# Kernel optimization log

Measured on AMD Instinct MI355X. Metric: run time of the kernel, lower is better.

Reference implementation:

```python
import jax, jax.numpy as jnp
import numpy as np

N = 50000      # nodes
E = 320000     # edges
D_NODE = 256   # node feature size
D_EDGE = 128   # raw edge feature size
T_DIM = 64     # time encoder out_channels
H = 8          # heads (auto_num_heads(256) -> 8)
C = 32         # per-head dim = 256 // 8
D_E_IN = D_EDGE + T_DIM  # edge_dim into lin_edge


def setup_inputs() -> dict:
    key = jax.random.key(0)
    ks = jax.random.split(key, 16)
    s_n = 1.0 / np.sqrt(D_NODE)
    s_e = 1.0 / np.sqrt(D_E_IN)
    return {
        "edge_tuples": jax.random.randint(ks[0], (2, E), 0, N, dtype=jnp.int64)
        if jax.config.jax_enable_x64 else jax.random.randint(ks[0], (2, E), 0, N),
        "edge_feats": jax.random.normal(ks[1], (E, D_EDGE), jnp.float32),
        "edge_times_rel": jax.random.uniform(ks[2], (E,), jnp.float32) * 100.0,
        "node_feats": jax.random.normal(ks[3], (N, D_NODE), jnp.float32),
        # time encoder: Linear(1, T_DIM) followed by cos
        "w_time": jax.random.normal(ks[4], (T_DIM,), jnp.float32),
        "b_time": jax.random.normal(ks[5], (T_DIM,), jnp.float32),
        # TransformerConv linears (out = H*C = 256)
        "Wq": jax.random.normal(ks[6], (H * C, D_NODE), jnp.float32) * s_n,
        "bq": jnp.zeros((H * C,), jnp.float32),
        "Wk": jax.random.normal(ks[7], (H * C, D_NODE), jnp.float32) * s_n,
        "bk": jnp.zeros((H * C,), jnp.float32),
        "Wv": jax.random.normal(ks[8], (H * C, D_NODE), jnp.float32) * s_n,
        "bv": jnp.zeros((H * C,), jnp.float32),
        "We": jax.random.normal(ks[9], (H * C, D_E_IN), jnp.float32) * s_e,  # lin_edge, no bias
        "Ws": jax.random.normal(ks[10], (H * C, D_NODE), jnp.float32) * s_n,  # lin_skip
        "bs": jnp.zeros((H * C,), jnp.float32),
    }


def reference(edge_tuples, edge_feats, edge_times_rel, node_feats,
              w_time, b_time, Wq, bq, Wk, bk, Wv, bv, We, Ws, bs):
    n_nodes = node_feats.shape[0]
    n_edges = edge_tuples.shape[1]
    src, dst = edge_tuples[0], edge_tuples[1]

    # TGN time encoder: cos(t * w + b)  -> [E, T_DIM]
    tfeat = jnp.cos(edge_times_rel[:, None] * w_time[None, :] + b_time)
    e_attr = jnp.concatenate([tfeat, edge_feats], axis=1)  # [E, T_DIM + D_EDGE]

    # dense per-node projections, then gather per edge
    q = (node_feats @ Wq.T + bq)[dst].reshape(n_edges, H, C)
    k = (node_feats @ Wk.T + bk)[src].reshape(n_edges, H, C)
    v = (node_feats @ Wv.T + bv)[src].reshape(n_edges, H, C)
    ep = (e_attr @ We.T).reshape(n_edges, H, C)

    k = k + ep
    alpha = jnp.sum(q * k, axis=-1) / jnp.sqrt(jnp.asarray(C, q.dtype))  # [E, H]

    # segment softmax over edges grouped by destination node
    m = jax.ops.segment_max(alpha, dst, num_segments=n_nodes)  # [N, H]
    m = jnp.where(jnp.isfinite(m), m, 0.0)
    ea = jnp.exp(alpha - m[dst])
    denom = jax.ops.segment_sum(ea, dst, num_segments=n_nodes)
    a = ea / (denom[dst] + 1e-16)  # [E, H]

    # weighted scatter-aggregate of (value + edge) messages
    msg = a[:, :, None] * (v + ep)  # [E, H, C]
    out = jax.ops.segment_sum(msg, dst, num_segments=n_nodes).reshape(n_nodes, H * C)

    # root / skip connection
    out = out + node_feats @ Ws.T + bs
    return out
```

## Files before the change

### kernel.cpp

```cpp
#include <hip/hip_runtime.h>
#include <hip/hip_bf16.h>
#include <math.h>

#define NN 50000
#define NE 320000
#define SCAN_NBLK ((NN + 255) / 256)

typedef __attribute__((ext_vector_type(8))) short bf16x8;
typedef __attribute__((ext_vector_type(4))) float floatx4;
typedef __attribute__((ext_vector_type(4))) unsigned int uintx4;

static __device__ __forceinline__ unsigned pack2bf(float a, float b) {
    __hip_bfloat162 h = __float22bfloat162_rn(make_float2(a, b));
    return *reinterpret_cast<unsigned*>(&h);
}
static __device__ __forceinline__ unsigned short f2bf(float x) {
    __hip_bfloat16 h = __float2bfloat16(x);
    return *reinterpret_cast<unsigned short*>(&h);
}
static __device__ __forceinline__ float bf2f(unsigned short u) {
    return __uint_as_float(((unsigned)u) << 16);
}
static __device__ __forceinline__ float bflo(unsigned u) {
    return __uint_as_float(u << 16);
}
static __device__ __forceinline__ float bfhi(unsigned u) {
    return __uint_as_float(u & 0xffff0000u);
}
static __device__ __forceinline__ void gload_lds16(const void* g, void* l) {
    __builtin_amdgcn_global_load_lds(
        (const __attribute__((address_space(1))) void*)g,
        (__attribute__((address_space(3))) void*)l, 16, 0, 0);
}

__global__ __launch_bounds__(256)
void cvt_bf16_kernel(const float* __restrict__ in,
                     unsigned short* __restrict__ out, int n8)
{
    int t = blockIdx.x * 256 + threadIdx.x;
    if (t >= n8) return;
    const float4* p = (const float4*)in + (size_t)t * 2;
    float4 a = p[0], b = p[1];
    uint4 u;
    u.x = pack2bf(a.x, a.y); u.y = pack2bf(a.z, a.w);
    u.z = pack2bf(b.x, b.y); u.w = pack2bf(b.z, b.w);
    ((uint4*)out)[t] = u;
}

__global__ __launch_bounds__(256)
void node_gemm_kernel(const unsigned short* __restrict__ Xb,
                      const unsigned short* __restrict__ Wqb,
                      const unsigned short* __restrict__ Wkb,
                      const unsigned short* __restrict__ Wvb,
                      const unsigned short* __restrict__ Wsb,
                      const float* __restrict__ bq, const float* __restrict__ bk,
                      const float* __restrict__ bv, const float* __restrict__ bs,
                      unsigned short* __restrict__ qb,
                      unsigned short* __restrict__ kb,
                      unsigned short* __restrict__ vb,
                      float* __restrict__ outS)
{
    const int m0  = blockIdx.x * 128;
    const int ct  = blockIdx.y;
    const int mat = ct >> 1, half = ct & 1;
    const int colbase = half * 128;

    const unsigned short* __restrict__ W;
    const float* __restrict__ bias;
    switch (mat) {
        case 0:  W = Wqb; bias = bq; break;
        case 1:  W = Wkb; bias = bk; break;
        case 2:  W = Wvb; bias = bv; break;
        default: W = Wsb; bias = bs; break;
    }
    W += (size_t)colbase * 256;

    __shared__ __align__(16) unsigned char smem[32768];
    short* sA = (short*)smem;
    short* sB = (short*)(smem + 16384);

    const int tid  = threadIdx.x;
    const int lane = tid & 63;
    const int wave = tid >> 6;
    const int wm   = (wave & 1) * 64;
    const int wn   = (wave >> 1) * 64;
    const int lr   = lane & 15;
    const int lq   = lane >> 4;

    const int srow = tid >> 3;
    const int scol = (tid & 7) * 8;

    floatx4 acc[4][4];
    #pragma unroll
    for (int i = 0; i < 4; ++i)
        #pragma unroll
        for (int j = 0; j < 4; ++j)
            acc[i][j] = (floatx4){0.f, 0.f, 0.f, 0.f};

    for (int k0 = 0; k0 < 256; k0 += 64) {
        #pragma unroll
        for (int p = 0; p < 4; ++p) {
            int arow = m0 + p * 32 + srow;
            if (arow > NN - 1) arow = NN - 1;
            gload_lds16(Xb + (size_t)arow * 256 + k0 + scol,
                        (char*)sA + p * 4096 + wave * 1024);
            gload_lds16(W + (size_t)(p * 32 + srow) * 256 + k0 + scol,
                        (char*)sB + p * 4096 + wave * 1024);
        }
        __syncthreads();

        #pragma unroll
        for (int ks = 0; ks < 2; ++ks) {
            bf16x8 af[4], bfr[4];
            #pragma unroll
            for (int i = 0; i < 4; ++i)
                af[i] = *(const bf16x8*)&sA[(wm + i * 16 + lr) * 64 + ks * 32 + lq * 8];
            #pragma unroll
            for (int j = 0; j < 4; ++j)
                bfr[j] = *(const bf16x8*)&sB[(wn + j * 16 + lr) * 64 + ks * 32 + lq * 8];
            #pragma unroll
            for (int i = 0; i < 4; ++i)
                #pragma unroll
                for (int j = 0; j < 4; ++j)
                    acc[i][j] = __builtin_amdgcn_mfma_f32_16x16x32_bf16(
                        af[i], bfr[j], acc[i][j], 0, 0, 0);
        }
        __syncthreads();
    }

    if (mat < 3) {
        unsigned short* __restrict__ Cb = (mat == 0) ? qb : (mat == 1) ? kb : vb;
        unsigned short* sOut = (unsigned short*)smem;
        for (int ch = 0; ch < 4; ++ch) {
            __syncthreads();
            if ((ch >> 1) == (wave & 1)) {
                int ibase = (ch & 1) * 2;
                #pragma unroll
                for (int ii = 0; ii < 2; ++ii) {
                    int i = ibase + ii;
                    #pragma unroll
                    for (int j = 0; j < 4; ++j) {
                        int col = wn + j * 16 + lr;
                        float bb = bias[colbase + col];
                        #pragma unroll
                        for (int r = 0; r < 4; ++r) {
                            int rowc = ii * 16 + lq * 4 + r;
                            sOut[rowc * 136 + col] = f2bf(acc[i][j][r] + bb);
                        }
                    }
                }
            }
            __syncthreads();
            #pragma unroll
            for (int p = 0; p < 2; ++p) {
                int rowc = p * 16 + (tid >> 4);
                int off  = (tid & 15) * 8;
                int grow = m0 + ch * 32 + rowc;
                if (grow < NN) {
                    uint4 u = *(const uint4*)&sOut[rowc * 136 + off];
                    *(uint4*)&Cb[(size_t)grow * 256 + colbase + off] = u;
                }
            }
        }
    } else {
        float* sOutF = (float*)smem;
        for (int ch = 0; ch < 8; ++ch) {
            __syncthreads();
            if ((ch >> 2) == (wave & 1)) {
                int i = ch & 3;
                #pragma unroll
                for (int j = 0; j < 4; ++j) {
                    int col = wn + j * 16 + lr;
                    float bb = bias[colbase + col];
                    #pragma unroll
                    for (int r = 0; r < 4; ++r) {
                        int rowc = lq * 4 + r;
                        sOutF[rowc * 132 + col] = acc[i][j][r] + bb;
                    }
                }
            }
            __syncthreads();
            #pragma unroll
            for (int p = 0; p < 2; ++p) {
                int rowc = p * 8 + (tid >> 5);
                int off  = (tid & 31) * 4;
                int grow = m0 + ch * 16 + rowc;
                if (grow < NN) {
                    float4 f = *(const float4*)&sOutF[rowc * 132 + off];
                    *(float4*)&outS[(size_t)grow * 256 + colbase + off] = f;
                }
            }
        }
    }
}

__global__ __launch_bounds__(256)
void edge_gemm_kernel(const float* __restrict__ tvals,
                      const float* __restrict__ w_time,
                      const float* __restrict__ b_time,
                      const float* __restrict__ ef,
                      const unsigned short* __restrict__ Web,
                      unsigned short* __restrict__ epb)
{
    const int m0 = blockIdx.x * 128;
    const int n0 = blockIdx.y * 128;

    __shared__ __align__(16) unsigned char smem[32768];
    short* sA = (short*)smem;
    short* sB = (short*)(smem + 16384);

    const int tid  = threadIdx.x;
    const int lane = tid & 63;
    const int wave = tid >> 6;
    const int wm   = (wave & 1) * 64;
    const int wn   = (wave >> 1) * 64;
    const int lr   = lane & 15;
    const int lq   = lane >> 4;

    const int srow = tid >> 3;
    const int scol = (tid & 7) * 8;

    floatx4 acc[4][4];
    #pragma unroll
    for (int i = 0; i < 4; ++i)
        #pragma unroll
        for (int j = 0; j < 4; ++j)
            acc[i][j] = (floatx4){0.f, 0.f, 0.f, 0.f};

    for (int k0 = 0; k0 < 192; k0 += 64) {
        #pragma unroll
        for (int p = 0; p < 4; ++p)
            gload_lds16(Web + (size_t)(n0 + p * 32 + srow) * 192 + k0 + scol,
                        (char*)sB + p * 4096 + wave * 1024);

        if (k0 == 0) {
            float w8[8], b8[8];
            #pragma unroll
            for (int j = 0; j < 8; ++j) {
                w8[j] = w_time[scol + j];
                b8[j] = b_time[scol + j];
            }
            #pragma unroll
            for (int p = 0; p < 4; ++p) {
                float tvv = tvals[m0 + p * 32 + srow];
                unsigned pk[4];
                #pragma unroll
                for (int j = 0; j < 4; ++j) {
                    float a = cosf(fmaf(tvv, w8[2 * j],     b8[2 * j]));
                    float b = cosf(fmaf(tvv, w8[2 * j + 1], b8[2 * j + 1]));
                    pk[j] = pack2bf(a, b);
                }
                *(uint4*)&sA[p * 2048 + tid * 8] = make_uint4(pk[0], pk[1], pk[2], pk[3]);
            }
        } else {
            float4 f[8];
            #pragma unroll
            for (int p = 0; p < 4; ++p) {
                const float4* src = (const float4*)(ef
                    + (size_t)(m0 + p * 32 + srow) * 128 + (k0 - 64) + scol);
                f[2 * p]     = src[0];
                f[2 * p + 1] = src[1];
            }
            #pragma unroll
            for (int p = 0; p < 4; ++p) {
                uint4 u;
                u.x = pack2bf(f[2 * p].x,     f[2 * p].y);
                u.y = pack2bf(f[2 * p].z,     f[2 * p].w);
                u.z = pack2bf(f[2 * p + 1].x, f[2 * p + 1].y);
                u.w = pack2bf(f[2 * p + 1].z, f[2 * p + 1].w);
                *(uint4*)&sA[p * 2048 + tid * 8] = u;
            }
        }
        __syncthreads();

        #pragma unroll
        for (int ks = 0; ks < 2; ++ks) {
            bf16x8 af[4], bfr[4];
            #pragma unroll
            for (int i = 0; i < 4; ++i)
                af[i] = *(const bf16x8*)&sA[(wm + i * 16 + lr) * 64 + ks * 32 + lq * 8];
            #pragma unroll
            for (int j = 0; j < 4; ++j)
                bfr[j] = *(const bf16x8*)&sB[(wn + j * 16 + lr) * 64 + ks * 32 + lq * 8];
            #pragma unroll
            for (int i = 0; i < 4; ++i)
                #pragma unroll
                for (int j = 0; j < 4; ++j)
                    acc[i][j] = __builtin_amdgcn_mfma_f32_16x16x32_bf16(
                        af[i], bfr[j], acc[i][j], 0, 0, 0);
        }
        __syncthreads();
    }

    unsigned short* sOut = (unsigned short*)smem;
    for (int ch = 0; ch < 4; ++ch) {
        __syncthreads();
        if ((ch >> 1) == (wave & 1)) {
            int ibase = (ch & 1) * 2;
            #pragma unroll
            for (int ii = 0; ii < 2; ++ii) {
                int i = ibase + ii;
                #pragma unroll
                for (int j = 0; j < 4; ++j) {
                    int col = wn + j * 16 + lr;
                    #pragma unroll
                    for (int r = 0; r < 4; ++r) {
                        int rowc = ii * 16 + lq * 4 + r;
                        sOut[rowc * 136 + col] = f2bf(acc[i][j][r]);
                    }
                }
            }
        }
        __syncthreads();
        #pragma unroll
        for (int p = 0; p < 2; ++p) {
            int rowc = p * 16 + (tid >> 4);
            int off  = (tid & 15) * 8;
            int grow = m0 + ch * 32 + rowc;
            uint4 u = *(const uint4*)&sOut[rowc * 136 + off];
            *(uint4*)&epb[(size_t)grow * 256 + n0 + off] = u;
        }
    }
}

__global__ __launch_bounds__(256)
void deg_kernel(const int* __restrict__ et, int* __restrict__ deg)
{
    int e = blockIdx.x * 256 + threadIdx.x;
    if (e < NE) atomicAdd(&deg[et[NE + e]], 1);
}

__global__ __launch_bounds__(256)
void blocksum_kernel(const int* __restrict__ deg, int* __restrict__ bsum)
{
    int idx = blockIdx.x * 256 + threadIdx.x;
    int v = (idx < NN) ? deg[idx] : 0;
    #pragma unroll
    for (int off = 1; off < 64; off <<= 1) v += __shfl_xor(v, off);
    __shared__ int s[4];
    if ((threadIdx.x & 63) == 0) s[threadIdx.x >> 6] = v;
    __syncthreads();
    if (threadIdx.x == 0) bsum[blockIdx.x] = s[0] + s[1] + s[2] + s[3];
}

__global__ __launch_bounds__(256)
void bscan_kernel(int* __restrict__ bsum, int* __restrict__ rowstart)
{
    __shared__ int s[256];
    int t = threadIdx.x;
    int v = (t < SCAN_NBLK) ? bsum[t] : 0;
    s[t] = v;
    __syncthreads();
    #pragma unroll
    for (int off = 1; off < 256; off <<= 1) {
        int u = (t >= off) ? s[t - off] : 0;
        __syncthreads();
        s[t] += u;
        __syncthreads();
    }
    if (t < SCAN_NBLK) bsum[t] = (t == 0) ? 0 : s[t - 1];
    if (t == 0) rowstart[NN] = s[SCAN_NBLK - 1];
}

__global__ __launch_bounds__(256)
void chunkscan_kernel(const int* __restrict__ deg, const int* __restrict__ bsum,
                      int* __restrict__ rowstart, int* __restrict__ cursor)
{
    __shared__ int s[256];
    int t = threadIdx.x;
    int idx = blockIdx.x * 256 + t;
    int v = (idx < NN) ? deg[idx] : 0;
    s[t] = v;
    __syncthreads();
    #pragma unroll
    for (int off = 1; off < 256; off <<= 1) {
        int u = (t >= off) ? s[t - off] : 0;
        __syncthreads();
        s[t] += u;
        __syncthreads();
    }
    if (idx < NN) {
        int ex = bsum[blockIdx.x] + s[t] - v;
        rowstart[idx] = ex;
        cursor[idx]   = ex;
    }
}

__global__ __launch_bounds__(256)
void scatter_kernel(const int* __restrict__ et,
                    int* __restrict__ cursor,
                    int2* __restrict__ eslist)
{
    int e = blockIdx.x * 256 + threadIdx.x;
    if (e < NE) {
        int d   = et[NE + e];
        int pos = atomicAdd(&cursor[d], 1);
        eslist[pos] = make_int2(e, et[e]);
    }
}

static __device__ __forceinline__ void edge_proc(
    uint4 ku, uint4 vu, uintx4 eu, const float* q, float mask,
    float* a, float& accd)
{
    float pe0 = bflo(eu[0]), pe1 = bfhi(eu[0]);
    float pe2 = bflo(eu[1]), pe3 = bfhi(eu[1]);
    float pe4 = bflo(eu[2]), pe5 = bfhi(eu[2]);
    float pe6 = bflo(eu[3]), pe7 = bfhi(eu[3]);

    float part;
    part = q[0] * (bflo(ku.x) + pe0);
    part = fmaf(q[1], bfhi(ku.x) + pe1, part);
    part = fmaf(q[2], bflo(ku.y) + pe2, part);
    part = fmaf(q[3], bfhi(ku.y) + pe3, part);
    part = fmaf(q[4], bflo(ku.z) + pe4, part);
    part = fmaf(q[5], bfhi(ku.z) + pe5, part);
    part = fmaf(q[6], bflo(ku.w) + pe6, part);
    part = fmaf(q[7], bfhi(ku.w) + pe7, part);
    part += __shfl_xor(part, 1);
    part += __shfl_xor(part, 2);

    float ea = __expf(part * 0.17677669529663687f) * mask;

    a[0] = fmaf(ea, bflo(vu.x) + pe0, a[0]);
    a[1] = fmaf(ea, bfhi(vu.x) + pe1, a[1]);
    a[2] = fmaf(ea, bflo(vu.y) + pe2, a[2]);
    a[3] = fmaf(ea, bfhi(vu.y) + pe3, a[3]);
    a[4] = fmaf(ea, bflo(vu.z) + pe4, a[4]);
    a[5] = fmaf(ea, bfhi(vu.z) + pe5, a[5]);
    a[6] = fmaf(ea, bflo(vu.w) + pe6, a[6]);
    a[7] = fmaf(ea, bfhi(vu.w) + pe7, a[7]);
    accd += ea;
}

__global__ __launch_bounds__(256)
void fused_agg_kernel(const int2* __restrict__ eslist,
                      const int* __restrict__ rowstart,
                      const unsigned short* __restrict__ qb,
                      const unsigned short* __restrict__ kb,
                      const unsigned short* __restrict__ vb,
                      const unsigned short* __restrict__ epb,
                      float* __restrict__ out)
{
    const int n = blockIdx.x * 4 + (threadIdx.x >> 6);
    if (n >= NN) return;
    const int lane = threadIdx.x & 63;
    const int half = lane >> 5;
    const int co   = (lane & 31) * 8;

    uint4 qu = *(const uint4*)(qb + (size_t)n * 256 + co);
    float q[8] = { bflo(qu.x), bfhi(qu.x), bflo(qu.y), bfhi(qu.y),
                   bflo(qu.z), bfhi(qu.z), bflo(qu.w), bfhi(qu.w) };

    float a[8] = {0.f, 0.f, 0.f, 0.f, 0.f, 0.f, 0.f, 0.f};
    float accd = 0.f;

    const int s0 = rowstart[n];
    const int s1 = rowstart[n + 1];

    int i = s0;
    for (; i + 4 <= s1; i += 4) {
        const int2 pA = eslist[i + half];
        const int2 pB = eslist[i + 2 + half];
        uint4 kA = *(const uint4*)(kb + (size_t)pA.y * 256 + co);
        uint4 vA = *(const uint4*)(vb + (size_t)pA.y * 256 + co);
        uintx4 eA = __builtin_nontemporal_load(
                        (const uintx4*)(epb + (size_t)pA.x * 256 + co));
        uint4 kB = *(const uint4*)(kb + (size_t)pB.y * 256 + co);
        uint4 vB = *(const uint4*)(vb + (size_t)pB.y * 256 + co);
        uintx4 eB = __builtin_nontemporal_load(
                        (const uintx4*)(epb + (size_t)pB.x * 256 + co));

        edge_proc(kA, vA, eA, q, 1.f, a, accd);
        edge_proc(kB, vB, eB, q, 1.f, a, accd);
    }
    for (; i + 2 <= s1; i += 2) {
        const int2 pA = eslist[i + half];
        uint4 kA = *(const uint4*)(kb + (size_t)pA.y * 256 + co);
        uint4 vA = *(const uint4*)(vb + (size_t)pA.y * 256 + co);
        uintx4 eA = __builtin_nontemporal_load(
                        (const uintx4*)(epb + (size_t)pA.x * 256 + co));
        edge_proc(kA, vA, eA, q, 1.f, a, accd);
    }
    if (i < s1) {
        int idx = i + half;
        float mask = (idx < s1) ? 1.f : 0.f;
        if (idx >= s1) idx = s1 - 1;
        const int2 pA = eslist[idx];
        uint4 kA = *(const uint4*)(kb + (size_t)pA.y * 256 + co);
        uint4 vA = *(const uint4*)(vb + (size_t)pA.y * 256 + co);
        uintx4 eA = __builtin_nontemporal_load(
                        (const uintx4*)(epb + (size_t)pA.x * 256 + co));
        edge_proc(kA, vA, eA, q, mask, a, accd);
    }

    #pragma unroll
    for (int j = 0; j < 8; ++j) a[j] += __shfl_xor(a[j], 32);
    accd += __shfl_xor(accd, 32);

    if (half == 0) {
        const float inv = 1.f / (accd + 1e-16f);
        float* po = out + (size_t)n * 256 + co;
        float4 o0 = ((const float4*)po)[0];
        float4 o1 = ((const float4*)po)[1];
        o0.x = fmaf(a[0], inv, o0.x);
        o0.y = fmaf(a[1], inv, o0.y);
        o0.z = fmaf(a[2], inv, o0.z);
        o0.w = fmaf(a[3], inv, o0.w);
        o1.x = fmaf(a[4], inv, o1.x);
        o1.y = fmaf(a[5], inv, o1.y);
        o1.z = fmaf(a[6], inv, o1.z);
        o1.w = fmaf(a[7], inv, o1.w);
        ((float4*)po)[0] = o0;
        ((float4*)po)[1] = o1;
    }
}

extern "C" void kernel_launch(void* const* d_in, const int* in_sizes, int n_in,
                              void* d_out, int out_size, void* d_ws, size_t ws_size,
                              hipStream_t stream)
{
    const int*   et  = (const int*)  d_in[0];
    const float* ef  = (const float*)d_in[1];
    const float* tv  = (const float*)d_in[2];
    const float* nf  = (const float*)d_in[3];
    const float* w_t = (const float*)d_in[4];
    const float* b_t = (const float*)d_in[5];
    const float* Wq  = (const float*)d_in[6];
    const float* bq  = (const float*)d_in[7];
    const float* Wk  = (const float*)d_in[8];
    const float* bk  = (const float*)d_in[9];
    const float* Wv  = (const float*)d_in[10];
    const float* bv  = (const float*)d_in[11];
    const float* We  = (const float*)d_in[12];
    const float* Ws  = (const float*)d_in[13];
    const float* bs  = (const float*)d_in[14];
    float* out = (float*)d_out;

    unsigned short* qb  = (unsigned short*)d_ws;
    unsigned short* kb  = qb  + (size_t)NN * 256;
    unsigned short* vb  = kb  + (size_t)NN * 256;
    unsigned short* epb = vb  + (size_t)NN * 256;
    unsigned short* nfb = epb + (size_t)NE * 256;
    unsigned short* Wqb = nfb + (size_t)NN * 256;
    unsigned short* Wkb = Wqb + 65536;
    unsigned short* Wvb = Wkb + 65536;
    unsigned short* Wsb = Wvb + 65536;
    unsigned short* Web = Wsb + 65536;
    int* deg      = (int*)(Web + 49152);
    int* rowstart = deg + NN;
    int* cursor   = rowstart + NN + 1;
    int2* eslist  = (int2*)(cursor + NN);
    int* bsum     = (int*)(eslist + NE);
    size_t need   = (size_t)((char*)(bsum + SCAN_NBLK) - (char*)d_ws);
    if (ws_size < need) return;

    (void)hipMemsetAsync(deg, 0, (size_t)NN * sizeof(int), stream);

    cvt_bf16_kernel<<<(NN * 256 / 8 + 255) / 256, 256, 0, stream>>>(nf, nfb, NN * 256 / 8);
    cvt_bf16_kernel<<<32, 256, 0, stream>>>(Wq, Wqb, 8192);
    cvt_bf16_kernel<<<32, 256, 0, stream>>>(Wk, Wkb, 8192);
    cvt_bf16_kernel<<<32, 256, 0, stream>>>(Wv, Wvb, 8192);
    cvt_bf16_kernel<<<32, 256, 0, stream>>>(Ws, Wsb, 8192);
    cvt_bf16_kernel<<<24, 256, 0, stream>>>(We, Web, 6144);

    node_gemm_kernel<<<dim3((NN + 127) / 128, 8), 256, 0, stream>>>(
        nfb, Wqb, Wkb, Wvb, Wsb, bq, bk, bv, bs, qb, kb, vb, out);

    edge_gemm_kernel<<<dim3(NE / 128, 2), 256, 0, stream>>>(
        tv, w_t, b_t, ef, Web, epb);

    deg_kernel<<<(NE + 255) / 256, 256, 0, stream>>>(et, deg);
    blocksum_kernel<<<SCAN_NBLK, 256, 0, stream>>>(deg, bsum);
    bscan_kernel<<<1, 256, 0, stream>>>(bsum, rowstart);
    chunkscan_kernel<<<SCAN_NBLK, 256, 0, stream>>>(deg, bsum, rowstart, cursor);
    scatter_kernel<<<(NE + 255) / 256, 256, 0, stream>>>(et, cursor, eslist);

    fused_agg_kernel<<<(NN + 3) / 4, 256, 0, stream>>>(
        eslist, rowstart, qb, kb, vb, epb, out);
}
```

Measured before the change: 586.1 us.

## Compute full edge projection width per block to avoid duplicate A-tile work

The edge GEMM now uses one 512-thread block per 128-edge tile that produces all 256 output columns, replacing two 256-thread blocks that each produced half. Before, both blocks recomputed the cosine time encoding and re-read and re-converted the fp32 edge features. That doubled the main memory traffic and transcendental work for the A operand. In exchange, each block uses more LDS (48 KB) and twice as many threads, which may lower occupancy and lengthen per-block barriers.

Result: no change. 579.0 us (-1.2%).

```diff
diff --git a/kernel.cpp b/kernel.cpp
--- a/kernel.cpp
+++ b/kernel.cpp
@@ -194,7 +194,7 @@
     }
 }
 
-__global__ __launch_bounds__(256)
+__global__ __launch_bounds__(512)
 void edge_gemm_kernel(const float* __restrict__ tvals,
                       const float* __restrict__ w_time,
                       const float* __restrict__ b_time,
@@ -203,9 +203,8 @@
                       unsigned short* __restrict__ epb)
 {
     const int m0 = blockIdx.x * 128;
-    const int n0 = blockIdx.y * 128;
-
-    __shared__ __align__(16) unsigned char smem[32768];
+
+    __shared__ __align__(16) unsigned char smem[49152];
     short* sA = (short*)smem;
     short* sB = (short*)(smem + 16384);
 
@@ -217,9 +216,6 @@
     const int lr   = lane & 15;
     const int lq   = lane >> 4;
 
-    const int srow = tid >> 3;
-    const int scol = (tid & 7) * 8;
-
     floatx4 acc[4][4];
     #pragma unroll
     for (int i = 0; i < 4; ++i)
@@ -230,45 +226,43 @@
     for (int k0 = 0; k0 < 192; k0 += 64) {
         #pragma unroll
         for (int p = 0; p < 4; ++p)
-            gload_lds16(Web + (size_t)(n0 + p * 32 + srow) * 192 + k0 + scol,
-                        (char*)sB + p * 4096 + wave * 1024);
+            gload_lds16(Web + (size_t)(p * 64 + (tid >> 3)) * 192 + k0 + (tid & 7) * 8,
+                        (char*)sB + p * 8192 + wave * 1024);
 
         if (k0 == 0) {
-            float w8[8], b8[8];
-            #pragma unroll
-            for (int j = 0; j < 8; ++j) {
-                w8[j] = w_time[scol + j];
-                b8[j] = b_time[scol + j];
-            }
-            #pragma unroll
-            for (int p = 0; p < 4; ++p) {
-                float tvv = tvals[m0 + p * 32 + srow];
-                unsigned pk[4];
-                #pragma unroll
-                for (int j = 0; j < 4; ++j) {
-                    float a = cosf(fmaf(tvv, w8[2 * j],     b8[2 * j]));
-                    float b = cosf(fmaf(tvv, w8[2 * j + 1], b8[2 * j + 1]));
-                    pk[j] = pack2bf(a, b);
-                }
-                *(uint4*)&sA[p * 2048 + tid * 8] = make_uint4(pk[0], pk[1], pk[2], pk[3]);
+            #pragma unroll
+            for (int p = 0; p < 2; ++p) {
+                int   row = p * 64 + (tid >> 3);
+                float tvv = tvals[m0 + row];
+                int   c0  = (tid & 7) * 8;
+                float4 w0 = *(const float4*)(w_time + c0);
+                float4 w1 = *(const float4*)(w_time + c0 + 4);
+                float4 b0 = *(const float4*)(b_time + c0);
+                float4 b1 = *(const float4*)(b_time + c0 + 4);
+                uint4 u;
+                u.x = pack2bf(cosf(fmaf(tvv, w0.x, b0.x)), cosf(fmaf(tvv, w0.y, b0.y)));
+                u.y = pack2bf(cosf(fmaf(tvv, w0.z, b0.z)), cosf(fmaf(tvv, w0.w, b0.w)));
+                u.z = pack2bf(cosf(fmaf(tvv, w1.x, b1.x)), cosf(fmaf(tvv, w1.y, b1.y)));
+                u.w = pack2bf(cosf(fmaf(tvv, w1.z, b1.z)), cosf(fmaf(tvv, w1.w, b1.w)));
+                *(uint4*)&sA[p * 4096 + tid * 8] = u;
             }
         } else {
-            float4 f[8];
-            #pragma unroll
-            for (int p = 0; p < 4; ++p) {
+            float4 f[4];
+            #pragma unroll
+            for (int p = 0; p < 2; ++p) {
                 const float4* src = (const float4*)(ef
-                    + (size_t)(m0 + p * 32 + srow) * 128 + (k0 - 64) + scol);
+                    + (size_t)(m0 + p * 64 + (tid >> 3)) * 128 + (k0 - 64) + (tid & 7) * 8);
                 f[2 * p]     = src[0];
                 f[2 * p + 1] = src[1];
             }
             #pragma unroll
-            for (int p = 0; p < 4; ++p) {
+            for (int p = 0; p < 2; ++p) {
                 uint4 u;
                 u.x = pack2bf(f[2 * p].x,     f[2 * p].y);
                 u.y = pack2bf(f[2 * p].z,     f[2 * p].w);
                 u.z = pack2bf(f[2 * p + 1].x, f[2 * p + 1].y);
                 u.w = pack2bf(f[2 * p + 1].z, f[2 * p + 1].w);
-                *(uint4*)&sA[p * 2048 + tid * 8] = u;
+                *(uint4*)&sA[p * 4096 + tid * 8] = u;
             }
         }
         __syncthreads();
@@ -295,7 +289,7 @@
     unsigned short* sOut = (unsigned short*)smem;
     for (int ch = 0; ch < 4; ++ch) {
         __syncthreads();
-        if ((ch >> 1) == (wave & 1)) {
+        if ((wave & 1) == (ch >> 1)) {
             int ibase = (ch & 1) * 2;
             #pragma unroll
             for (int ii = 0; ii < 2; ++ii) {
@@ -306,7 +300,7 @@
                     #pragma unroll
                     for (int r = 0; r < 4; ++r) {
                         int rowc = ii * 16 + lq * 4 + r;
-                        sOut[rowc * 136 + col] = f2bf(acc[i][j][r]);
+                        sOut[rowc * 264 + col] = f2bf(acc[i][j][r]);
                     }
                 }
             }
@@ -314,11 +308,11 @@
         __syncthreads();
         #pragma unroll
         for (int p = 0; p < 2; ++p) {
-            int rowc = p * 16 + (tid >> 4);
-            int off  = (tid & 15) * 8;
-            int grow = m0 + ch * 32 + rowc;
-            uint4 u = *(const uint4*)&sOut[rowc * 136 + off];
-            *(uint4*)&epb[(size_t)grow * 256 + n0 + off] = u;
+            int rl   = p * 16 + (tid >> 5);
+            int off  = (tid & 31) * 8;
+            int grow = m0 + ch * 32 + rl;
+            uint4 u = *(const uint4*)&sOut[rl * 264 + off];
+            *(uint4*)&epb[(size_t)grow * 256 + off] = u;
         }
     }
 }
@@ -567,7 +561,7 @@
     node_gemm_kernel<<<dim3((NN + 127) / 128, 8), 256, 0, stream>>>(
         nfb, Wqb, Wkb, Wvb, Wsb, bq, bk, bv, bs, qb, kb, vb, out);
 
-    edge_gemm_kernel<<<dim3(NE / 128, 2), 256, 0, stream>>>(
+    edge_gemm_kernel<<<NE / 128, 512, 0, stream>>>(
         tv, w_t, b_t, ef, Web, epb);
 
     deg_kernel<<<(NE + 255) / 256, 256, 0, stream>>>(et, deg);
```
